# Kernel optimization log

Hardware: AMD Instinct MI355X
Metric: run time of the kernel (lower is better)

The kernel has to match this reference:

```python
import jax, jax.numpy as jnp
import numpy as np

N = 40000
IN_DIM = 128
HID = 64
E = 640000


def sage_conv(x, edge_index, W_l, b_l, W_r):
    """PyG SAGEConv with mean aggregation.
    out = lin_l(mean_{j in N(i)} x_j) + lin_r(x_i)
    edge_index[0]=src (message source), edge_index[1]=dst (aggregation target).
    """
    src, dst = edge_index[0], edge_index[1]
    n = x.shape[0]
    msgs = x[src]                                            # [E, d] gather
    sums = jax.ops.segment_sum(msgs, dst, num_segments=n)    # [N, d]
    cnt = jax.ops.segment_sum(jnp.ones((msgs.shape[0],), x.dtype), dst,
                              num_segments=n)                # [N]
    mean = sums / jnp.maximum(cnt, 1.0)[:, None]
    return mean @ W_l.T + b_l + x @ W_r.T


def setup_inputs() -> dict:
    key = jax.random.key(0)
    ks = jax.random.split(key, 8)
    x = jax.random.normal(ks[0], (N, IN_DIM), dtype=jnp.float32)
    edge_index = jax.random.randint(ks[1], (2, E), 0, N, dtype=jnp.int32)
    s1 = 1.0 / np.sqrt(IN_DIM)
    s2 = 1.0 / np.sqrt(HID)
    W1_l = jax.random.uniform(ks[2], (HID, IN_DIM), jnp.float32, -s1, s1)
    b1_l = jax.random.uniform(ks[3], (HID,), jnp.float32, -s1, s1)
    W1_r = jax.random.uniform(ks[4], (HID, IN_DIM), jnp.float32, -s1, s1)
    W2_l = jax.random.uniform(ks[5], (HID, HID), jnp.float32, -s2, s2)
    b2_l = jax.random.uniform(ks[6], (HID,), jnp.float32, -s2, s2)
    W2_r = jax.random.uniform(ks[7], (HID, HID), jnp.float32, -s2, s2)
    return {"x": x, "edge_index": edge_index,
            "W1_l": W1_l, "b1_l": b1_l, "W1_r": W1_r,
            "W2_l": W2_l, "b2_l": b2_l, "W2_r": W2_r}


def reference(x, edge_index, W1_l, b1_l, W1_r, W2_l, b2_l, W2_r):
    h = sage_conv(x, edge_index, W1_l, b1_l, W1_r)
    h = jax.nn.relu(h)
    # dropout is identity in eval mode (reference baseline is deterministic)
    z = sage_conv(h, edge_index, W2_l, b2_l, W2_r)
    return z
```

## Files before the change

### kernel.cpp

```cpp
#include <hip/hip_runtime.h>

#define INDIM 128
#define HID 64
#define CAP 64
#define GEMM_BLOCKS 625
#define BIN_BLOCKS 256
#define PREP_BLOCKS 32
#define RSH 7
#define RMASK ((1 << RSH) - 1)
#define NRANGE 313
#define SBCAP 28

__device__ __forceinline__ float bf2f(unsigned short u) {
    union { unsigned int i; float f; } c; c.i = ((unsigned int)u) << 16; return c.f;
}
__device__ __forceinline__ unsigned short f2bf(float f) {
    union { float f; unsigned int i; } c; c.f = f;
    return (unsigned short)((c.i + 0x7FFFu + ((c.i >> 16) & 1u)) >> 16);
}

__device__ __forceinline__ void agg8(const unsigned short* __restrict__ Pb,
                                     int idx0, int deg, int q, int f8,
                                     float acc[8]) {
    const int nstep = (deg + 7) >> 3;
    for (int s = 0; s < nstep; s += 2) {
        #pragma unroll
        for (int u = 0; u < 2; ++u) {
            const int ss = s + u;
            const int lanesel = ss * 8 + q;
            const int sidx = __shfl(idx0, lanesel, 64);
            const float m = (ss < nstep && lanesel < deg) ? 1.f : 0.f;
            const uint4 v = *(const uint4*)&Pb[(size_t)sidx * 64 + f8 * 8];
            acc[0] += bf2f((unsigned short)(v.x & 0xffffu)) * m;
            acc[1] += bf2f((unsigned short)(v.x >> 16)) * m;
            acc[2] += bf2f((unsigned short)(v.y & 0xffffu)) * m;
            acc[3] += bf2f((unsigned short)(v.y >> 16)) * m;
            acc[4] += bf2f((unsigned short)(v.z & 0xffffu)) * m;
            acc[5] += bf2f((unsigned short)(v.z >> 16)) * m;
            acc[6] += bf2f((unsigned short)(v.w & 0xffffu)) * m;
            acc[7] += bf2f((unsigned short)(v.w >> 16)) * m;
        }
    }
    #pragma unroll
    for (int j = 0; j < 8; ++j) {
        acc[j] += __shfl_xor(acc[j], 8, 64);
        acc[j] += __shfl_xor(acc[j], 16, 64);
        acc[j] += __shfl_xor(acc[j], 32, 64);
    }
}


__global__ __launch_bounds__(256) void k_bin_prep(
    const int* __restrict__ src, const int* __restrict__ dst,
    unsigned int* __restrict__ hist_global, unsigned int* __restrict__ ebin,
    const float* __restrict__ W1l, const float* __restrict__ W1r,
    const float* __restrict__ W2l, const float* __restrict__ W2r,
    float* __restrict__ WT1l, float* __restrict__ WT1r,
    float* __restrict__ WT2l, float* __restrict__ WT2r, int E) {
    const int tid = threadIdx.x;

    if (blockIdx.x >= BIN_BLOCKS) {
        const int gtid = (blockIdx.x - BIN_BLOCKS) * 256 + tid;
        if (gtid < 64 * 128) {
            int j = gtid >> 7, k = gtid & 127;
            WT1l[k * 64 + j] = W1l[gtid];
            WT1r[k * 64 + j] = W1r[gtid];
        }
        if (gtid < 64 * 64) {
            int j = gtid >> 6, k = gtid & 63;
            WT2l[k * 64 + j] = W2l[gtid];
            WT2r[k * 64 + j] = W2r[gtid];
        }
        return;
    }

    __shared__ unsigned int hist[NRANGE];
    __shared__ unsigned int cur[NRANGE];
    const int b = blockIdx.x;
    const int ech = (E + BIN_BLOCKS - 1) / BIN_BLOCKS;
    const int e0 = b * ech;
    const int e1 = (e0 + ech < E) ? e0 + ech : E;

    for (int r = tid; r < NRANGE; r += 256) { hist[r] = 0; cur[r] = 0; }
    __syncthreads();
    for (int e = e0 + tid; e < e1; e += 256)
        atomicAdd(&hist[((unsigned)dst[e]) >> RSH], 1u);
    __syncthreads();
    for (int r = tid; r < NRANGE; r += 256)
        hist_global[(size_t)r * BIN_BLOCKS + b] = hist[r];
    __syncthreads();
    for (int e = e0 + tid; e < e1; e += 256) {
        const unsigned d = (unsigned)dst[e];
        const unsigned s = (unsigned)src[e];
        const unsigned r = d >> RSH;
        const unsigned off = atomicAdd(&cur[r], 1u);
        if (off < SBCAP)
            ebin[((size_t)r * BIN_BLOCKS + b) * SBCAP + off] = (d << 16) | s;
    }
}


__global__ __launch_bounds__(256) void k_gemm1_place(
    const float* __restrict__ A,
    const float* __restrict__ WTl, const float* __restrict__ WTr,
    unsigned short* __restrict__ Pb, float* __restrict__ Q,
    const unsigned int* __restrict__ hist_global,
    const unsigned int* __restrict__ ebin,
    int* __restrict__ cnt, unsigned short* __restrict__ sorted, int N) {
    __shared__ float As[64][INDIM + 1];
    __shared__ unsigned int lcnt[1 << RSH];
    const int tid = threadIdx.x;

    if (blockIdx.x < NRANGE) {
        const int r = blockIdx.x;
        if (tid < (1 << RSH)) lcnt[tid] = 0;
        __syncthreads();
        unsigned c = hist_global[(size_t)r * BIN_BLOCKS + tid];
        if (c > SBCAP) c = SBCAP;
        const unsigned int* eb = ebin + ((size_t)r * BIN_BLOCKS + tid) * SBCAP;
        for (unsigned i = 0; i < c; ++i) {
            const unsigned p = eb[i];
            const unsigned d = p >> 16;
            const unsigned slot = atomicAdd(&lcnt[d & RMASK], 1u);
            if (slot < CAP)
                sorted[(d << 6) + slot] = (unsigned short)(p & 0xffffu);
        }
        __syncthreads();
        for (int l = tid; l < (1 << RSH); l += 256) {
            const int node = (r << RSH) + l;
            if (node < N) cnt[node] = (int)lcnt[l];
        }
        return;
    }

    const int bm = (blockIdx.x - NRANGE) * 64;
    for (int idx = tid; idx < 64 * 32; idx += 256) {
        int row = idx >> 5, kq = idx & 31;
        const float4 v = ((const float4*)A)[(size_t)(bm + row) * 32 + kq];
        As[row][kq * 4 + 0] = v.x; As[row][kq * 4 + 1] = v.y;
        As[row][kq * 4 + 2] = v.z; As[row][kq * 4 + 3] = v.w;
    }
    __syncthreads();

    const int tx = tid & 15, ty = tid >> 4;
    const int n0 = ty * 4;
    float accl[4][4] = {}, accr[4][4] = {};
    #pragma unroll 8
    for (int k = 0; k < INDIM; ++k) {
        float a[4];
        #pragma unroll
        for (int i = 0; i < 4; ++i) a[i] = As[n0 + i][k];
        const float4 blv = ((const float4*)WTl)[k * 16 + tx];
        const float4 brv = ((const float4*)WTr)[k * 16 + tx];
        const float bl[4] = {blv.x, blv.y, blv.z, blv.w};
        const float br[4] = {brv.x, brv.y, brv.z, brv.w};
        #pragma unroll
        for (int i = 0; i < 4; ++i) {
            #pragma unroll
            for (int j = 0; j < 4; ++j) {
                accl[i][j] += a[i] * bl[j];
                accr[i][j] += a[i] * br[j];
            }
        }
    }
    #pragma unroll
    for (int i = 0; i < 4; ++i) {
        int m = bm + n0 + i;
        ushort4 pv;
        pv.x = f2bf(accl[i][0]); pv.y = f2bf(accl[i][1]);
        pv.z = f2bf(accl[i][2]); pv.w = f2bf(accl[i][3]);
        ((ushort4*)Pb)[(size_t)m * 16 + tx] = pv;
        ((float4*)Q)[(size_t)m * 16 + tx] =
            make_float4(accr[i][0], accr[i][1], accr[i][2], accr[i][3]);
    }
}


__global__ __launch_bounds__(512) void k_agg1_gemm2(
    const unsigned short* __restrict__ Pb, const float* __restrict__ Q,
    const float* __restrict__ b1,
    const int* __restrict__ cnt, const unsigned short* __restrict__ sorted,
    const float* __restrict__ WTl, const float* __restrict__ WTr,
    unsigned short* __restrict__ Pb2, float* __restrict__ Q2, int N) {
    __shared__ float Hs[64][HID + 4];
    const int tid = threadIdx.x;
    const int bm = blockIdx.x * 64;
    const int lane = tid & 63, w = tid >> 6;
    const int q = lane >> 3, f8 = lane & 7;
    const int node_base = bm + w * 8;

    int degv = (lane < 8 && node_base + lane < N) ? cnt[node_base + lane] : 0;
    int degs[8], idx0s[8];
    #pragma unroll
    for (int r = 0; r < 8; ++r) {
        int d = __shfl(degv, r, 64);
        d = (d > CAP) ? CAP : d;
        degs[r] = d;
        const int ls = (lane < d) ? lane : ((d > 0) ? d - 1 : 0);
        idx0s[r] = (d > 0) ? (int)sorted[((node_base + r) << 6) + ls] : 0;
    }

    #pragma unroll
    for (int r = 0; r < 8; ++r) {
        const int node = node_base + r;
        if (node >= N) break;
        float acc[8] = {};
        agg8(Pb, idx0s[r], degs[r], q, f8, acc);
        if (q == 0) {
            const float inv = 1.0f / fmaxf((float)degs[r], 1.0f);
            const float4 qa = *(const float4*)&Q[(size_t)node * 64 + f8 * 8];
            const float4 qb = *(const float4*)&Q[(size_t)node * 64 + f8 * 8 + 4];
            const float4 ba = *(const float4*)&b1[f8 * 8];
            const float4 bb = *(const float4*)&b1[f8 * 8 + 4];
            float4 h0, h1;
            h0.x = fmaxf(acc[0] * inv + ba.x + qa.x, 0.f);
            h0.y = fmaxf(acc[1] * inv + ba.y + qa.y, 0.f);
            h0.z = fmaxf(acc[2] * inv + ba.z + qa.z, 0.f);
            h0.w = fmaxf(acc[3] * inv + ba.w + qa.w, 0.f);
            h1.x = fmaxf(acc[4] * inv + bb.x + qb.x, 0.f);
            h1.y = fmaxf(acc[5] * inv + bb.y + qb.y, 0.f);
            h1.z = fmaxf(acc[6] * inv + bb.z + qb.z, 0.f);
            h1.w = fmaxf(acc[7] * inv + bb.w + qb.w, 0.f);
            *(float4*)&Hs[w * 8 + r][f8 * 8] = h0;
            *(float4*)&Hs[w * 8 + r][f8 * 8 + 4] = h1;
        }
    }
    __syncthreads();

    const int tx = tid & 15, ty = tid >> 4;
    const int n0 = ty * 2;
    float accl[2][4] = {}, accr[2][4] = {};
    #pragma unroll 8
    for (int k = 0; k < HID; ++k) {
        float a[2];
        #pragma unroll
        for (int i = 0; i < 2; ++i) a[i] = Hs[n0 + i][k];
        const float4 blv = ((const float4*)WTl)[k * 16 + tx];
        const float4 brv = ((const float4*)WTr)[k * 16 + tx];
        const float bl[4] = {blv.x, blv.y, blv.z, blv.w};
        const float br[4] = {brv.x, brv.y, brv.z, brv.w};
        #pragma unroll
        for (int i = 0; i < 2; ++i) {
            #pragma unroll
            for (int j = 0; j < 4; ++j) {
                accl[i][j] += a[i] * bl[j];
                accr[i][j] += a[i] * br[j];
            }
        }
    }
    #pragma unroll
    for (int i = 0; i < 2; ++i) {
        int m = bm + n0 + i;
        if (m < N) {
            ushort4 pv;
            pv.x = f2bf(accl[i][0]); pv.y = f2bf(accl[i][1]);
            pv.z = f2bf(accl[i][2]); pv.w = f2bf(accl[i][3]);
            ((ushort4*)Pb2)[(size_t)m * 16 + tx] = pv;
            ((float4*)Q2)[(size_t)m * 16 + tx] =
                make_float4(accr[i][0], accr[i][1], accr[i][2], accr[i][3]);
        }
    }
}


__global__ __launch_bounds__(256) void k_agg2(
    const unsigned short* __restrict__ Pb2, const float* __restrict__ Q2,
    const float* __restrict__ b2,
    const int* __restrict__ cnt, const unsigned short* __restrict__ sorted,
    float* __restrict__ z, int N) {
    const int wid  = (blockIdx.x * 256 + threadIdx.x) >> 6;
    const int lane = threadIdx.x & 63;
    const int q = lane >> 3, f8 = lane & 7;
    if (wid >= N) return;
    int deg = cnt[wid]; if (deg > CAP) deg = CAP;
    const int ls = (lane < deg) ? lane : ((deg > 0) ? deg - 1 : 0);
    const int idx0 = (deg > 0) ? (int)sorted[(wid << 6) + ls] : 0;
    float acc[8] = {};
    agg8(Pb2, idx0, deg, q, f8, acc);
    if (q == 0) {
        const float inv = 1.0f / fmaxf((float)deg, 1.0f);
        const float4 qa = *(const float4*)&Q2[(size_t)wid * 64 + f8 * 8];
        const float4 qb = *(const float4*)&Q2[(size_t)wid * 64 + f8 * 8 + 4];
        const float4 ba = *(const float4*)&b2[f8 * 8];
        const float4 bb = *(const float4*)&b2[f8 * 8 + 4];
        float4 z0, z1;
        z0.x = acc[0] * inv + ba.x + qa.x;
        z0.y = acc[1] * inv + ba.y + qa.y;
        z0.z = acc[2] * inv + ba.z + qa.z;
        z0.w = acc[3] * inv + ba.w + qa.w;
        z1.x = acc[4] * inv + bb.x + qb.x;
        z1.y = acc[5] * inv + bb.y + qb.y;
        z1.z = acc[6] * inv + bb.z + qb.z;
        z1.w = acc[7] * inv + bb.w + qb.w;
        *(float4*)&z[(size_t)wid * 64 + f8 * 8] = z0;
        *(float4*)&z[(size_t)wid * 64 + f8 * 8 + 4] = z1;
    }
}


extern "C" void kernel_launch(void* const* d_in, const int* in_sizes, int n_in,
                              void* d_out, int out_size, void* d_ws, size_t ws_size,
                              hipStream_t stream) {
    const float* x   = (const float*)d_in[0];
    const int*  edge = (const int*)d_in[1];
    const float* W1l = (const float*)d_in[2];
    const float* b1l = (const float*)d_in[3];
    const float* W1r = (const float*)d_in[4];
    const float* W2l = (const float*)d_in[5];
    const float* b2l = (const float*)d_in[6];
    const float* W2r = (const float*)d_in[7];

    const int N = in_sizes[0] / INDIM;
    const int E = in_sizes[1] / 2;
    const int* src = edge;
    const int* dst = edge + E;

    char* w = (char*)d_ws;
    auto carve = [&](size_t bytes) {
        char* p = w; w += (bytes + 255) & ~(size_t)255; return p;
    };
    unsigned short* Pb  = (unsigned short*)carve((size_t)N * 64 * 2);
    unsigned short* Pb2 = (unsigned short*)carve((size_t)N * 64 * 2);
    float* Q    = (float*)carve((size_t)N * 64 * 4);
    float* Q2   = (float*)carve((size_t)N * 64 * 4);
    float* WT1l = (float*)carve(128 * 64 * 4);
    float* WT1r = (float*)carve(128 * 64 * 4);
    float* WT2l = (float*)carve(64 * 64 * 4);
    float* WT2r = (float*)carve(64 * 64 * 4);
    int* cnt    = (int*)carve((size_t)N * 4);
    unsigned short* sorted = (unsigned short*)carve((size_t)N * CAP * 2);
    unsigned int* hist_global = (unsigned int*)carve((size_t)NRANGE * BIN_BLOCKS * 4);
    unsigned int* ebin = (unsigned int*)carve((size_t)NRANGE * BIN_BLOCKS * SBCAP * 4);

    float* zout = (float*)d_out;

    const int gT = (N + 63) / 64;
    const int gW = (N * 64 + 255) / 256;

    k_bin_prep<<<BIN_BLOCKS + PREP_BLOCKS, 256, 0, stream>>>(
        src, dst, hist_global, ebin,
        W1l, W1r, W2l, W2r, WT1l, WT1r, WT2l, WT2r, E);
    k_gemm1_place<<<NRANGE + GEMM_BLOCKS, 256, 0, stream>>>(
        x, WT1l, WT1r, Pb, Q, hist_global, ebin, cnt, sorted, N);
    k_agg1_gemm2<<<gT, 512, 0, stream>>>(Pb, Q, b1l, cnt, sorted,
                                         WT2l, WT2r, Pb2, Q2, N);
    k_agg2<<<gW, 256, 0, stream>>>(Pb2, Q2, b2l, cnt, sorted, zout, N);
}
```

Measured before the change: 108.3 us.

## Reorder layer-two SAGEConv to aggregate hidden features before applying the linear transform

Layer two switches from transform-then-aggregate to aggregate-then-transform. The fused agg1+gemm2 kernel is split into three kernels: agg1 writes H in both bf16 and fp32, agg2h gathers the bf16 H and writes the neighbour mean, and a new GEMM kernel computes meanH·Wl + H·Wr + b. This frees the aggregation kernels from the GEMM's shared-memory and occupancy limits. In exchange it adds one kernel launch and extra global round-trips for H and meanH in fp32, and the layer-two transform now runs on bf16-rounded H for the aggregated term.

```diff
diff --git a/kernel.cpp b/kernel.cpp
--- a/kernel.cpp
+++ b/kernel.cpp
@@ -176,98 +176,11 @@
 }
 
 
-__global__ __launch_bounds__(512) void k_agg1_gemm2(
+__global__ __launch_bounds__(256) void k_agg1(
     const unsigned short* __restrict__ Pb, const float* __restrict__ Q,
     const float* __restrict__ b1,
     const int* __restrict__ cnt, const unsigned short* __restrict__ sorted,
-    const float* __restrict__ WTl, const float* __restrict__ WTr,
-    unsigned short* __restrict__ Pb2, float* __restrict__ Q2, int N) {
-    __shared__ float Hs[64][HID + 4];
-    const int tid = threadIdx.x;
-    const int bm = blockIdx.x * 64;
-    const int lane = tid & 63, w = tid >> 6;
-    const int q = lane >> 3, f8 = lane & 7;
-    const int node_base = bm + w * 8;
-
-    int degv = (lane < 8 && node_base + lane < N) ? cnt[node_base + lane] : 0;
-    int degs[8], idx0s[8];
-    #pragma unroll
-    for (int r = 0; r < 8; ++r) {
-        int d = __shfl(degv, r, 64);
-        d = (d > CAP) ? CAP : d;
-        degs[r] = d;
-        const int ls = (lane < d) ? lane : ((d > 0) ? d - 1 : 0);
-        idx0s[r] = (d > 0) ? (int)sorted[((node_base + r) << 6) + ls] : 0;
-    }
-
-    #pragma unroll
-    for (int r = 0; r < 8; ++r) {
-        const int node = node_base + r;
-        if (node >= N) break;
-        float acc[8] = {};
-        agg8(Pb, idx0s[r], degs[r], q, f8, acc);
-        if (q == 0) {
-            const float inv = 1.0f / fmaxf((float)degs[r], 1.0f);
-            const float4 qa = *(const float4*)&Q[(size_t)node * 64 + f8 * 8];
-            const float4 qb = *(const float4*)&Q[(size_t)node * 64 + f8 * 8 + 4];
-            const float4 ba = *(const float4*)&b1[f8 * 8];
-            const float4 bb = *(const float4*)&b1[f8 * 8 + 4];
-            float4 h0, h1;
-            h0.x = fmaxf(acc[0] * inv + ba.x + qa.x, 0.f);
-            h0.y = fmaxf(acc[1] * inv + ba.y + qa.y, 0.f);
-            h0.z = fmaxf(acc[2] * inv + ba.z + qa.z, 0.f);
-            h0.w = fmaxf(acc[3] * inv + ba.w + qa.w, 0.f);
-            h1.x = fmaxf(acc[4] * inv + bb.x + qb.x, 0.f);
-            h1.y = fmaxf(acc[5] * inv + bb.y + qb.y, 0.f);
-            h1.z = fmaxf(acc[6] * inv + bb.z + qb.z, 0.f);
-            h1.w = fmaxf(acc[7] * inv + bb.w + qb.w, 0.f);
-            *(float4*)&Hs[w * 8 + r][f8 * 8] = h0;
-            *(float4*)&Hs[w * 8 + r][f8 * 8 + 4] = h1;
-        }
-    }
-    __syncthreads();
-
-    const int tx = tid & 15, ty = tid >> 4;
-    const int n0 = ty * 2;
-    float accl[2][4] = {}, accr[2][4] = {};
-    #pragma unroll 8
-    for (int k = 0; k < HID; ++k) {
-        float a[2];
-        #pragma unroll
-        for (int i = 0; i < 2; ++i) a[i] = Hs[n0 + i][k];
-        const float4 blv = ((const float4*)WTl)[k * 16 + tx];
-        const float4 brv = ((const float4*)WTr)[k * 16 + tx];
-        const float bl[4] = {blv.x, blv.y, blv.z, blv.w};
-        const float br[4] = {brv.x, brv.y, brv.z, brv.w};
-        #pragma unroll
-        for (int i = 0; i < 2; ++i) {
-            #pragma unroll
-            for (int j = 0; j < 4; ++j) {
-                accl[i][j] += a[i] * bl[j];
-                accr[i][j] += a[i] * br[j];
-            }
-        }
-    }
-    #pragma unroll
-    for (int i = 0; i < 2; ++i) {
-        int m = bm + n0 + i;
-        if (m < N) {
-            ushort4 pv;
-            pv.x = f2bf(accl[i][0]); pv.y = f2bf(accl[i][1]);
-            pv.z = f2bf(accl[i][2]); pv.w = f2bf(accl[i][3]);
-            ((ushort4*)Pb2)[(size_t)m * 16 + tx] = pv;
-            ((float4*)Q2)[(size_t)m * 16 + tx] =
-                make_float4(accr[i][0], accr[i][1], accr[i][2], accr[i][3]);
-        }
-    }
-}
-
-
-__global__ __launch_bounds__(256) void k_agg2(
-    const unsigned short* __restrict__ Pb2, const float* __restrict__ Q2,
-    const float* __restrict__ b2,
-    const int* __restrict__ cnt, const unsigned short* __restrict__ sorted,
-    float* __restrict__ z, int N) {
+    unsigned short* __restrict__ Hb, float* __restrict__ H, int N) {
     const int wid  = (blockIdx.x * 256 + threadIdx.x) >> 6;
     const int lane = threadIdx.x & 63;
     const int q = lane >> 3, f8 = lane & 7;
@@ -276,24 +189,103 @@
     const int ls = (lane < deg) ? lane : ((deg > 0) ? deg - 1 : 0);
     const int idx0 = (deg > 0) ? (int)sorted[(wid << 6) + ls] : 0;
     float acc[8] = {};
-    agg8(Pb2, idx0, deg, q, f8, acc);
+    agg8(Pb, idx0, deg, q, f8, acc);
     if (q == 0) {
         const float inv = 1.0f / fmaxf((float)deg, 1.0f);
-        const float4 qa = *(const float4*)&Q2[(size_t)wid * 64 + f8 * 8];
-        const float4 qb = *(const float4*)&Q2[(size_t)wid * 64 + f8 * 8 + 4];
-        const float4 ba = *(const float4*)&b2[f8 * 8];
-        const float4 bb = *(const float4*)&b2[f8 * 8 + 4];
-        float4 z0, z1;
-        z0.x = acc[0] * inv + ba.x + qa.x;
-        z0.y = acc[1] * inv + ba.y + qa.y;
-        z0.z = acc[2] * inv + ba.z + qa.z;
-        z0.w = acc[3] * inv + ba.w + qa.w;
-        z1.x = acc[4] * inv + bb.x + qb.x;
-        z1.y = acc[5] * inv + bb.y + qb.y;
-        z1.z = acc[6] * inv + bb.z + qb.z;
-        z1.w = acc[7] * inv + bb.w + qb.w;
-        *(float4*)&z[(size_t)wid * 64 + f8 * 8] = z0;
-        *(float4*)&z[(size_t)wid * 64 + f8 * 8 + 4] = z1;
+        const float4 qa = *(const float4*)&Q[(size_t)wid * 64 + f8 * 8];
+        const float4 qb = *(const float4*)&Q[(size_t)wid * 64 + f8 * 8 + 4];
+        const float4 ba = *(const float4*)&b1[f8 * 8];
+        const float4 bb = *(const float4*)&b1[f8 * 8 + 4];
+        float h0 = fmaxf(acc[0] * inv + ba.x + qa.x, 0.f);
+        float h1 = fmaxf(acc[1] * inv + ba.y + qa.y, 0.f);
+        float h2 = fmaxf(acc[2] * inv + ba.z + qa.z, 0.f);
+        float h3 = fmaxf(acc[3] * inv + ba.w + qa.w, 0.f);
+        float h4 = fmaxf(acc[4] * inv + bb.x + qb.x, 0.f);
+        float h5 = fmaxf(acc[5] * inv + bb.y + qb.y, 0.f);
+        float h6 = fmaxf(acc[6] * inv + bb.z + qb.z, 0.f);
+        float h7 = fmaxf(acc[7] * inv + bb.w + qb.w, 0.f);
+        uint4 u;
+        u.x = (unsigned)f2bf(h0) | ((unsigned)f2bf(h1) << 16);
+        u.y = (unsigned)f2bf(h2) | ((unsigned)f2bf(h3) << 16);
+        u.z = (unsigned)f2bf(h4) | ((unsigned)f2bf(h5) << 16);
+        u.w = (unsigned)f2bf(h6) | ((unsigned)f2bf(h7) << 16);
+        *(uint4*)&Hb[(size_t)wid * 64 + f8 * 8] = u;
+        *(float4*)&H[(size_t)wid * 64 + f8 * 8] = make_float4(h0, h1, h2, h3);
+        *(float4*)&H[(size_t)wid * 64 + f8 * 8 + 4] = make_float4(h4, h5, h6, h7);
+    }
+}
+
+
+__global__ __launch_bounds__(256) void k_agg2h(
+    const unsigned short* __restrict__ Hb,
+    const int* __restrict__ cnt, const unsigned short* __restrict__ sorted,
+    float* __restrict__ meanH, int N) {
+    const int wid  = (blockIdx.x * 256 + threadIdx.x) >> 6;
+    const int lane = threadIdx.x & 63;
+    const int q = lane >> 3, f8 = lane & 7;
+    if (wid >= N) return;
+    int deg = cnt[wid]; if (deg > CAP) deg = CAP;
+    const int ls = (lane < deg) ? lane : ((deg > 0) ? deg - 1 : 0);
+    const int idx0 = (deg > 0) ? (int)sorted[(wid << 6) + ls] : 0;
+    float acc[8] = {};
+    agg8(Hb, idx0, deg, q, f8, acc);
+    if (q == 0) {
+        const float inv = 1.0f / fmaxf((float)deg, 1.0f);
+        *(float4*)&meanH[(size_t)wid * 64 + f8 * 8] =
+            make_float4(acc[0] * inv, acc[1] * inv, acc[2] * inv, acc[3] * inv);
+        *(float4*)&meanH[(size_t)wid * 64 + f8 * 8 + 4] =
+            make_float4(acc[4] * inv, acc[5] * inv, acc[6] * inv, acc[7] * inv);
+    }
+}
+
+
+__global__ __launch_bounds__(256) void k_gemm_z(
+    const float* __restrict__ meanH, const float* __restrict__ H,
+    const float* __restrict__ WTl, const float* __restrict__ WTr,
+    const float* __restrict__ b2, float* __restrict__ z, int N) {
+    __shared__ float As1[64][HID + 1];
+    __shared__ float As2[64][HID + 1];
+    const int tid = threadIdx.x;
+    const int bm = blockIdx.x * 64;
+    for (int idx = tid; idx < 64 * 16; idx += 256) {
+        int row = idx >> 4, kq = idx & 15;
+        const float4 v1 = ((const float4*)meanH)[(size_t)(bm + row) * 16 + kq];
+        const float4 v2 = ((const float4*)H)[(size_t)(bm + row) * 16 + kq];
+        As1[row][kq * 4 + 0] = v1.x; As1[row][kq * 4 + 1] = v1.y;
+        As1[row][kq * 4 + 2] = v1.z; As1[row][kq * 4 + 3] = v1.w;
+        As2[row][kq * 4 + 0] = v2.x; As2[row][kq * 4 + 1] = v2.y;
+        As2[row][kq * 4 + 2] = v2.z; As2[row][kq * 4 + 3] = v2.w;
+    }
+    __syncthreads();
+
+    const int tx = tid & 15, ty = tid >> 4;
+    const int n0 = ty * 4;
+    float acc[4][4] = {};
+    #pragma unroll 8
+    for (int k = 0; k < HID; ++k) {
+        float a1[4], a2[4];
+        #pragma unroll
+        for (int i = 0; i < 4; ++i) { a1[i] = As1[n0 + i][k]; a2[i] = As2[n0 + i][k]; }
+        const float4 blv = ((const float4*)WTl)[k * 16 + tx];
+        const float4 brv = ((const float4*)WTr)[k * 16 + tx];
+        const float bl[4] = {blv.x, blv.y, blv.z, blv.w};
+        const float br[4] = {brv.x, brv.y, brv.z, brv.w};
+        #pragma unroll
+        for (int i = 0; i < 4; ++i) {
+            #pragma unroll
+            for (int j = 0; j < 4; ++j)
+                acc[i][j] += a1[i] * bl[j] + a2[i] * br[j];
+        }
+    }
+    const float4 bv = *(const float4*)&b2[tx * 4];
+    #pragma unroll
+    for (int i = 0; i < 4; ++i) {
+        int m = bm + n0 + i;
+        if (m < N) {
+            ((float4*)z)[(size_t)m * 16 + tx] =
+                make_float4(acc[i][0] + bv.x, acc[i][1] + bv.y,
+                            acc[i][2] + bv.z, acc[i][3] + bv.w);
+        }
     }
 }
 
@@ -320,9 +312,10 @@
         char* p = w; w += (bytes + 255) & ~(size_t)255; return p;
     };
     unsigned short* Pb  = (unsigned short*)carve((size_t)N * 64 * 2);
-    unsigned short* Pb2 = (unsigned short*)carve((size_t)N * 64 * 2);
-    float* Q    = (float*)carve((size_t)N * 64 * 4);
-    float* Q2   = (float*)carve((size_t)N * 64 * 4);
+    unsigned short* Hb  = (unsigned short*)carve((size_t)N * 64 * 2);
+    float* Q     = (float*)carve((size_t)N * 64 * 4);
+    float* H     = (float*)carve((size_t)N * 64 * 4);
+    float* meanH = (float*)carve((size_t)N * 64 * 4);
     float* WT1l = (float*)carve(128 * 64 * 4);
     float* WT1r = (float*)carve(128 * 64 * 4);
     float* WT2l = (float*)carve(64 * 64 * 4);
@@ -342,7 +335,7 @@
         W1l, W1r, W2l, W2r, WT1l, WT1r, WT2l, WT2r, E);
     k_gemm1_place<<<NRANGE + GEMM_BLOCKS, 256, 0, stream>>>(
         x, WT1l, WT1r, Pb, Q, hist_global, ebin, cnt, sorted, N);
-    k_agg1_gemm2<<<gT, 512, 0, stream>>>(Pb, Q, b1l, cnt, sorted,
-                                         WT2l, WT2r, Pb2, Q2, N);
-    k_agg2<<<gW, 256, 0, stream>>>(Pb2, Q2, b2l, cnt, sorted, zout, N);
-}
+    k_agg1<<<gW, 256, 0, stream>>>(Pb, Q, b1l, cnt, sorted, Hb, H, N);
+    k_agg2h<<<gW, 256, 0, stream>>>(Hb, cnt, sorted, meanH, N);
+    k_gemm_z<<<gT, 256, 0, stream>>>(meanH, H, WT2l, WT2r, b2l, zout, N);
+}
```

New measurement: 109.9 us. No clear change (+1.5%).
